# Kernel optimization log

Hardware: AMD Instinct MI355X
Metric: run time of the kernel (lower is better)

Reference implementation:

```python
import jax, jax.numpy as jnp
import numpy as np

DIM = 768
N_HEADS = 12
HEAD_DIM = DIM // N_HEADS
MLP_DIM = 3072
DEPTH = 12
B, N = 16, 512


def setup_inputs() -> dict:
    key = jax.random.key(0)
    ks = jax.random.split(key, 12)
    s = 0.02
    return {
        "x": jax.random.normal(ks[0], (B, N, DIM), dtype=jnp.float32),
        "ln_w": jnp.ones((DIM,), jnp.float32),
        "ln_b": jnp.zeros((DIM,), jnp.float32),
        "wq": jax.random.normal(ks[1], (DIM, DIM), jnp.float32) * s,
        "bq": jnp.zeros((DIM,), jnp.float32),
        "wk": jax.random.normal(ks[2], (DIM, DIM), jnp.float32) * s,
        "bk": jnp.zeros((DIM,), jnp.float32),
        "wv": jax.random.normal(ks[3], (DIM, DIM), jnp.float32) * s,
        "bv": jnp.zeros((DIM,), jnp.float32),
        "w1": jax.random.normal(ks[4], (DIM, MLP_DIM), jnp.float32) * s,
        "b1": jnp.zeros((MLP_DIM,), jnp.float32),
        "w2": jax.random.normal(ks[5], (MLP_DIM, DIM), jnp.float32) * s,
        "b2": jnp.zeros((DIM,), jnp.float32),
    }


def _layernorm(x, w, b):
    mu = jnp.mean(x, axis=-1, keepdims=True)
    var = jnp.var(x, axis=-1, keepdims=True)
    return (x - mu) * jax.lax.rsqrt(var + 1e-5) * w + b


def _mha(x, wq, bq, wk, bk, wv, bv):
    # x: [b, n, dim]; weights stored as [in, out]
    def heads(t):
        return t.reshape(B, N, N_HEADS, HEAD_DIM).transpose(0, 2, 1, 3)  # b h n d
    q = heads(x @ wq + bq)
    k = heads(x @ wk + bk)
    v = heads(x @ wv + bv)
    scores = jnp.einsum('bhqd,bhkd->bhqk', q, k) / np.sqrt(HEAD_DIM).astype(np.float32)
    attn = jax.nn.softmax(scores, axis=-1)
    o = jnp.einsum('bhqk,bhkd->bhqd', attn, v)
    return o.transpose(0, 2, 1, 3).reshape(B, N, DIM)


def reference(x, ln_w, ln_b, wq, bq, wk, bk, wv, bv, w1, b1, w2, b2):
    # Dropout is identity in eval mode. Same weights reused each depth iteration.
    for _ in range(DEPTH):
        x = _mha(_layernorm(x, ln_w, ln_b), wq, bq, wk, bk, wv, bv) + x
        h = _layernorm(x, ln_w, ln_b)
        h = jax.nn.gelu(h @ w1 + b1, approximate=False) @ w2 + b2
        x = h + x
    return x
```

## Files before the change

kernel.cpp:

```cpp
#include <hip/hip_runtime.h>

typedef __bf16 bf16x8 __attribute__((ext_vector_type(8)));
typedef float f32x4 __attribute__((ext_vector_type(4)));
typedef unsigned short ushort8_t __attribute__((ext_vector_type(8)));
typedef unsigned short ushort4_t __attribute__((ext_vector_type(4)));

#define MFMA16(a, b, c) __builtin_amdgcn_mfma_f32_16x16x32_bf16((a), (b), (c), 0, 0, 0)

#define GLOAD16(gp, lp)                                                        \
  __builtin_amdgcn_global_load_lds(                                            \
      (__attribute__((address_space(1))) void*)(gp),                           \
      (__attribute__((address_space(3))) void*)(lp), 16, 0, 0)

__device__ __forceinline__ unsigned short f2bf(float f) {
  unsigned u = __builtin_bit_cast(unsigned, f);
  return (unsigned short)((u + 0x7FFFu + ((u >> 16) & 1u)) >> 16);
}

__global__ __launch_bounds__(256) void transpose_f2b(
    const float* __restrict__ src, unsigned short* __restrict__ dst,
    int Kdim, int Ndim) {
  long i = (long)blockIdx.x * 256 + threadIdx.x;
  if (i >= (long)Kdim * Ndim) return;
  int n = (int)(i / Kdim);
  int kk = (int)(i - (long)n * Kdim);
  dst[i] = f2bf(src[(long)kk * Ndim + n]);
}

__global__ __launch_bounds__(256) void ln_kernel(
    const float* __restrict__ x, const float* __restrict__ gw,
    const float* __restrict__ gb, unsigned short* __restrict__ h) {
  const int row = blockIdx.x * 4 + (threadIdx.x >> 6);
  const int l = threadIdx.x & 63;
  const float* xr = x + (long)row * 768;
  f32x4 va[3];
#pragma unroll
  for (int i = 0; i < 3; i++) va[i] = *(const f32x4*)(xr + i * 256 + l * 4);
  float s = 0.f, ss = 0.f;
#pragma unroll
  for (int i = 0; i < 3; i++)
#pragma unroll
    for (int j = 0; j < 4; j++) {
      float t = va[i][j];
      s += t;
      ss += t * t;
    }
#pragma unroll
  for (int off = 1; off < 64; off <<= 1) {
    s += __shfl_xor(s, off, 64);
    ss += __shfl_xor(ss, off, 64);
  }
  const float mu = s * (1.f / 768.f);
  const float var = ss * (1.f / 768.f) - mu * mu;
  const float inv = rsqrtf(var + 1e-5f);
  unsigned short* hp = h + (long)row * 768;
#pragma unroll
  for (int i = 0; i < 3; i++) {
    f32x4 wv = *(const f32x4*)(gw + i * 256 + l * 4);
    f32x4 bv = *(const f32x4*)(gb + i * 256 + l * 4);
    ushort4_t o;
#pragma unroll
    for (int j = 0; j < 4; j++) o[j] = f2bf((va[i][j] - mu) * inv * wv[j] + bv[j]);
    *(ushort4_t*)(hp + i * 256 + l * 4) = o;
  }
}

enum { EPI_QKV = 0, EPI_GELU = 1, EPI_RES = 2 };

template <int EPI, int MREP>
__global__ __launch_bounds__(256) void gemm_bt(
    const unsigned short* __restrict__ A, const unsigned short* __restrict__ BT,
    int K, const float* __restrict__ bb0, const float* __restrict__ bb1,
    const float* __restrict__ bb2, unsigned short* __restrict__ o0,
    unsigned short* __restrict__ o1, unsigned short* __restrict__ o2,
    const float* oFin, float* oFout) {
  constexpr int BM = MREP * 32;
  constexpr int ABUF = BM * 32;
  __shared__ unsigned short As[2][ABUF];
  __shared__ unsigned short Bs[2][128 * 32];
  const int tid = threadIdx.x;
  const int w = tid >> 6, l = tid & 63;
  const int lr = l & 15, lg = l >> 4;
  const int wr = w >> 1, wc = w & 1;
  const int fchunk = ((l & 3) ^ ((l >> 3) & 3)) * 8;
  const int sR = (lr >> 1) & 3;

  const int nx = gridDim.x;
  const int nwg = nx * gridDim.y;
  int wg = blockIdx.y * nx + blockIdx.x;
  {
    const int qq = nwg >> 3, rr = nwg & 7;
    const int xcd = wg & 7, idx = wg >> 3;
    wg = (xcd < rr ? xcd * (qq + 1) : rr * (qq + 1) + (xcd - rr) * qq) + idx;
  }
  const int bx = wg % nx, by = wg / nx;
  const int m0 = by * BM, n0 = bx * 128;

  const unsigned short* Ag =
      A + (long)(m0 + w * (BM / 4) + (l >> 2)) * K + fchunk;
  const unsigned short* Bg = BT + (long)(n0 + w * 32 + (l >> 2)) * K + fchunk;
  unsigned short* AsW = &As[0][w * (BM / 4) * 32 + l * 8];
  unsigned short* BsW = &Bs[0][w * 1024 + l * 8];

  auto stage = [&](int buf, int kt) {
    const unsigned short* ag = Ag + kt * 32;
    const unsigned short* bg = Bg + kt * 32;
    unsigned short* aw = AsW + buf * ABUF;
    unsigned short* bw = BsW + buf * 4096;
#pragma unroll
    for (int i = 0; i < BM / 64; i++) GLOAD16(ag + i * 16 * K, aw + i * 512);
    GLOAD16(bg, bw);
    GLOAD16(bg + 16 * K, bw + 512);
  };

  f32x4 acc[MREP][4] = {};
  const int nk = K >> 5;
  stage(0, 0);
  __syncthreads();
  for (int kt = 0; kt < nk; ++kt) {
    const int cur = kt & 1;
    if (kt + 1 < nk) stage(cur ^ 1, kt + 1);
    bf16x8 a[MREP], b[4];
#pragma unroll
    for (int i = 0; i < MREP; i++)
      a[i] = *(const bf16x8*)(&As[cur][(wr * MREP * 16 + i * 16 + lr) * 32 +
                                       ((lg ^ sR) * 8)]);
#pragma unroll
    for (int j = 0; j < 4; j++)
      b[j] = *(const bf16x8*)(&Bs[cur][(wc * 64 + j * 16 + lr) * 32 +
                                       ((lg ^ sR) * 8)]);
#pragma unroll
    for (int i = 0; i < MREP; i++)
#pragma unroll
      for (int j = 0; j < 4; j++) acc[i][j] = MFMA16(a[i], b[j], acc[i][j]);
    __syncthreads();
  }

  if (EPI == EPI_QKV) {
    const int whichq = n0 / 768;
    const int cc0 = n0 - whichq * 768;
    const float* bias = whichq == 0 ? bb0 : whichq == 1 ? bb1 : bb2;
    if (whichq < 2) {
      unsigned short* dst = whichq == 0 ? o0 : o1;
#pragma unroll
      for (int i = 0; i < MREP; i++) {
        const int r = m0 + wr * MREP * 16 + i * 16 + lg * 4;
#pragma unroll
        for (int j = 0; j < 4; j++) {
          const int ccol = cc0 + wc * 64 + j * 16 + lr;
          const int hd = ccol >> 6, d = ccol & 63;
          const float bv = bias[ccol];
#pragma unroll
          for (int q = 0; q < 4; q++) {
            const int row = r + q;
            const int bidx = row >> 9, n = row & 511;
            const long addr = ((long)(bidx * 12 + hd) * 512 + n) * 64 + d;
            dst[addr] = f2bf(acc[i][j][q] + bv);
          }
        }
      }
    } else {
#pragma unroll
      for (int i = 0; i < MREP; i++) {
        const int r = m0 + wr * MREP * 16 + i * 16 + lg * 4;
        const int bidx = r >> 9, n = r & 511;
#pragma unroll
        for (int j = 0; j < 4; j++) {
          const int ccol = cc0 + wc * 64 + j * 16 + lr;
          const int hd = ccol >> 6, d = ccol & 63;
          const float bv = bias[ccol];
          ushort4_t pk;
#pragma unroll
          for (int q = 0; q < 4; q++) pk[q] = f2bf(acc[i][j][q] + bv);
          *(ushort4_t*)(&o2[((long)(bidx * 12 + hd) * 64 + d) * 512 + n]) = pk;
        }
      }
    }
  } else if (EPI == EPI_GELU) {
#pragma unroll
    for (int i = 0; i < MREP; i++) {
      const int r = m0 + wr * MREP * 16 + i * 16 + lg * 4;
#pragma unroll
      for (int j = 0; j < 4; j++) {
        const int c = n0 + wc * 64 + j * 16 + lr;
        const float bv = bb0[c];
#pragma unroll
        for (int q = 0; q < 4; q++) {
          float v = acc[i][j][q] + bv;
          const float u = v * (0.7978845608f + 0.0356774081f * v * v);
          const float g = v / (1.0f + __expf(-2.0f * u));
          o0[(long)(r + q) * 3072 + c] = f2bf(g);
        }
      }
    }
  } else {
#pragma unroll
    for (int i = 0; i < MREP; i++) {
      const int r = m0 + wr * MREP * 16 + i * 16 + lg * 4;
#pragma unroll
      for (int j = 0; j < 4; j++) {
        const int c = n0 + wc * 64 + j * 16 + lr;
        const float bv = bb0[c];
#pragma unroll
        for (int q = 0; q < 4; q++) {
          const long addr = (long)(r + q) * 768 + c;
          oFout[addr] = acc[i][j][q] + bv + oFin[addr];
        }
      }
    }
  }
}

__global__ __launch_bounds__(256) void attn_kernel(
    const unsigned short* __restrict__ qg, const unsigned short* __restrict__ kg,
    const unsigned short* __restrict__ vtg, float* __restrict__ x) {
  __shared__ unsigned short Sh[128 * 64];
  __shared__ unsigned short Ks[2][64 * 64];
  __shared__ unsigned short Vt[2][64 * 64];
  const int qt = blockIdx.x, h = blockIdx.y, b = blockIdx.z;
  const int bh = b * 12 + h;
  const int tid = threadIdx.x, w = tid >> 6, l = tid & 63;
  const int lr = l & 15, lg = l >> 4;
  const int fchunk = ((l & 7) ^ ((l >> 3) & 7)) * 8;
  const int rk = lr & 7;

  const unsigned short* qbase =
      qg + ((long)bh * 512 + qt * 128 + w * 32 + (l >> 3)) * 64 + fchunk;
  unsigned short* shW = &Sh[w * 2048 + l * 8];
#pragma unroll
  for (int cc = 0; cc < 4; cc++) GLOAD16(qbase + cc * 8 * 64, shW + cc * 512);

  const unsigned short* kbase =
      kg + ((long)bh * 512 + w * 16 + (l >> 3)) * 64 + fchunk;
  const unsigned short* vbase =
      vtg + ((long)bh * 64 + w * 16 + (l >> 3)) * 512 + fchunk;
  unsigned short* KsW = &Ks[0][w * 1024 + l * 8];
  unsigned short* VtW = &Vt[0][w * 1024 + l * 8];

  auto stageKV = [&](int buf, int kt) {
#pragma unroll
    for (int cc = 0; cc < 2; cc++) {
      GLOAD16(kbase + (kt * 64 + cc * 8) * 64, KsW + buf * 4096 + cc * 512);
      GLOAD16(vbase + cc * 8 * 512 + kt * 64, VtW + buf * 4096 + cc * 512);
    }
  };
  stageKV(0, 0);
  __syncthreads();

  bf16x8 qa[2][2];
#pragma unroll
  for (int mi = 0; mi < 2; mi++)
#pragma unroll
    for (int ds = 0; ds < 2; ds++) {
      qa[mi][ds] = *(const bf16x8*)(&Sh[(w * 32 + mi * 16 + lr) * 64 +
                                        ((ds * 4 + lg) ^ rk) * 8]);
#pragma unroll
      for (int e = 0; e < 8; e++)
        qa[mi][ds][e] = (__bf16)(0.125f * (float)qa[mi][ds][e]);
    }

  unsigned short* Pw = &Sh[w * 2048];
  float lsum[8] = {};
  f32x4 o[2][4] = {};

  for (int kt = 0; kt < 8; ++kt) {
    const int cur = kt & 1;
    if (kt < 7) stageKV(cur ^ 1, kt + 1);

    f32x4 s[2][4] = {};
#pragma unroll
    for (int ds = 0; ds < 2; ++ds) {
      bf16x8 kb[4];
#pragma unroll
      for (int nj = 0; nj < 4; nj++)
        kb[nj] = *(const bf16x8*)(&Ks[cur][(nj * 16 + lr) * 64 +
                                           ((ds * 4 + lg) ^ rk) * 8]);
#pragma unroll
      for (int mi = 0; mi < 2; mi++)
#pragma unroll
        for (int nj = 0; nj < 4; nj++) s[mi][nj] = MFMA16(qa[mi][ds], kb[nj], s[mi][nj]);
    }

#pragma unroll
    for (int mi = 0; mi < 2; mi++)
#pragma unroll
      for (int nj = 0; nj < 4; nj++) {
        const int cL = nj * 2 + (lr >> 3);
#pragma unroll
        for (int q = 0; q < 4; q++) {
          const int row = mi * 16 + lg * 4 + q;
          const float p = __expf(s[mi][nj][q]);
          lsum[mi * 4 + q] += p;
          Pw[row * 64 + ((cL ^ (row & 7)) * 8) + (lr & 7)] = f2bf(p);
        }
      }

#pragma unroll
    for (int ks = 0; ks < 2; ++ks) {
      bf16x8 pa[2], vb[4];
#pragma unroll
      for (int mi = 0; mi < 2; mi++)
        pa[mi] = *(const bf16x8*)(&Pw[(mi * 16 + lr) * 64 +
                                      ((ks * 4 + lg) ^ rk) * 8]);
#pragma unroll
      for (int dj = 0; dj < 4; dj++)
        vb[dj] = *(const bf16x8*)(&Vt[cur][(dj * 16 + lr) * 64 +
                                           ((ks * 4 + lg) ^ rk) * 8]);
#pragma unroll
      for (int mi = 0; mi < 2; mi++)
#pragma unroll
        for (int dj = 0; dj < 4; dj++) o[mi][dj] = MFMA16(pa[mi], vb[dj], o[mi][dj]);
    }
    __syncthreads();
  }

#pragma unroll
  for (int i = 0; i < 8; i++) {
#pragma unroll
    for (int off = 1; off < 16; off <<= 1) lsum[i] += __shfl_xor(lsum[i], off, 64);
  }

#pragma unroll
  for (int mi = 0; mi < 2; mi++) {
#pragma unroll
    for (int q = 0; q < 4; q++) {
      const int n = qt * 128 + w * 32 + mi * 16 + lg * 4 + q;
      const float inv = 1.0f / lsum[mi * 4 + q];
      const long base = ((long)(b * 512 + n)) * 768 + h * 64;
#pragma unroll
      for (int dj = 0; dj < 4; dj++) {
        const long a = base + dj * 16 + lr;
        x[a] = x[a] + o[mi][dj][q] * inv;
      }
    }
  }
}

extern "C" void kernel_launch(void* const* d_in, const int* in_sizes, int n_in,
                              void* d_out, int out_size, void* d_ws,
                              size_t ws_size, hipStream_t stream) {
  const float* x_in = (const float*)d_in[0];
  const float* ln_w = (const float*)d_in[1];
  const float* ln_b = (const float*)d_in[2];
  const float* wq = (const float*)d_in[3];
  const float* bq = (const float*)d_in[4];
  const float* wk = (const float*)d_in[5];
  const float* bk = (const float*)d_in[6];
  const float* wv = (const float*)d_in[7];
  const float* bv = (const float*)d_in[8];
  const float* w1 = (const float*)d_in[9];
  const float* b1 = (const float*)d_in[10];
  const float* w2 = (const float*)d_in[11];
  const float* b2 = (const float*)d_in[12];

  char* p = (char*)d_ws;
  float* xw = (float*)p;            p += 8192L * 768 * 4;
  unsigned short* hbuf = (unsigned short*)p;  p += 8192L * 768 * 2;
  unsigned short* wqkvT = (unsigned short*)p; p += 2304L * 768 * 2;
  unsigned short* w1T = (unsigned short*)p;   p += 3072L * 768 * 2;
  unsigned short* w2T = (unsigned short*)p;   p += 768L * 3072 * 2;
  unsigned short* qb = (unsigned short*)p;
  unsigned short* kb = qb + 6291456L;
  unsigned short* vt = kb + 6291456L;
  unsigned short* gbuf = qb;

  hipMemcpyAsync(xw, x_in, 8192L * 768 * 4, hipMemcpyDeviceToDevice, stream);

  transpose_f2b<<<(768 * 768 + 255) / 256, 256, 0, stream>>>(wq, wqkvT, 768, 768);
  transpose_f2b<<<(768 * 768 + 255) / 256, 256, 0, stream>>>(wk, wqkvT + 589824L, 768, 768);
  transpose_f2b<<<(768 * 768 + 255) / 256, 256, 0, stream>>>(wv, wqkvT + 1179648L, 768, 768);
  transpose_f2b<<<(768 * 3072 + 255) / 256, 256, 0, stream>>>(w1, w1T, 768, 3072);
  transpose_f2b<<<(768 * 3072 + 255) / 256, 256, 0, stream>>>(w2, w2T, 3072, 768);

  for (int layer = 0; layer < 12; ++layer) {
    ln_kernel<<<2048, 256, 0, stream>>>(xw, ln_w, ln_b, hbuf);
    gemm_bt<EPI_QKV, 4><<<dim3(18, 64), 256, 0, stream>>>(
        hbuf, wqkvT, 768, bq, bk, bv, qb, kb, vt, nullptr, nullptr);
    attn_kernel<<<dim3(4, 12, 16), 256, 0, stream>>>(qb, kb, vt, xw);
    ln_kernel<<<2048, 256, 0, stream>>>(xw, ln_w, ln_b, hbuf);
    gemm_bt<EPI_GELU, 4><<<dim3(24, 64), 256, 0, stream>>>(
        hbuf, w1T, 768, b1, nullptr, nullptr, gbuf, nullptr, nullptr, nullptr,
        nullptr);
    gemm_bt<EPI_RES, 2><<<dim3(6, 128), 256, 0, stream>>>(
        gbuf, w2T, 3072, b2, nullptr, nullptr, nullptr, nullptr, nullptr, xw,
        layer == 11 ? (float*)d_out : xw);
  }
}
```

Measured before the change: 2.888 ms.

## Triple-buffer GEMM and attention LDS staging with vmcnt waits and single barrier

```diff
diff --git a/kernel.cpp b/kernel.cpp
--- a/kernel.cpp
+++ b/kernel.cpp
@@ -11,6 +11,12 @@
   __builtin_amdgcn_global_load_lds(                                            \
       (__attribute__((address_space(1))) void*)(gp),                           \
       (__attribute__((address_space(3))) void*)(lp), 16, 0, 0)
+
+#define WAITVM(N) asm volatile("s_waitcnt vmcnt(" #N ")" ::: "memory")
+__device__ __forceinline__ void barrier_fence() {
+  __builtin_amdgcn_s_barrier();
+  __builtin_amdgcn_sched_barrier(0);
+}
 
 __device__ __forceinline__ unsigned short f2bf(float f) {
   unsigned u = __builtin_bit_cast(unsigned, f);
@@ -76,8 +82,9 @@
     const float* oFin, float* oFout) {
   constexpr int BM = MREP * 32;
   constexpr int ABUF = BM * 32;
-  __shared__ unsigned short As[2][ABUF];
-  __shared__ unsigned short Bs[2][128 * 32];
+  constexpr int LPS = BM / 64 + 2;
+  __shared__ unsigned short As[3][ABUF];
+  __shared__ unsigned short Bs[3][128 * 32];
   const int tid = threadIdx.x;
   const int w = tid >> 6, l = tid & 63;
   const int lr = l & 15, lg = l >> 4;
@@ -99,14 +106,12 @@
   const unsigned short* Ag =
       A + (long)(m0 + w * (BM / 4) + (l >> 2)) * K + fchunk;
   const unsigned short* Bg = BT + (long)(n0 + w * 32 + (l >> 2)) * K + fchunk;
-  unsigned short* AsW = &As[0][w * (BM / 4) * 32 + l * 8];
-  unsigned short* BsW = &Bs[0][w * 1024 + l * 8];
 
   auto stage = [&](int buf, int kt) {
     const unsigned short* ag = Ag + kt * 32;
     const unsigned short* bg = Bg + kt * 32;
-    unsigned short* aw = AsW + buf * ABUF;
-    unsigned short* bw = BsW + buf * 4096;
+    unsigned short* aw = &As[buf][w * (BM / 4) * 32 + l * 8];
+    unsigned short* bw = &Bs[buf][w * 1024 + l * 8];
 #pragma unroll
     for (int i = 0; i < BM / 64; i++) GLOAD16(ag + i * 16 * K, aw + i * 512);
     GLOAD16(bg, bw);
@@ -116,10 +121,21 @@
   f32x4 acc[MREP][4] = {};
   const int nk = K >> 5;
   stage(0, 0);
-  __syncthreads();
+  stage(1, 1);
+  int cur = 0;
   for (int kt = 0; kt < nk; ++kt) {
-    const int cur = kt & 1;
-    if (kt + 1 < nk) stage(cur ^ 1, kt + 1);
+    if (kt + 2 < nk) {
+      if constexpr (LPS == 4) WAITVM(4); else WAITVM(3);
+      barrier_fence();
+      const int nxt = cur + 2 >= 3 ? cur - 1 : cur + 2;
+      stage(nxt, kt + 2);
+    } else if (kt + 1 < nk) {
+      if constexpr (LPS == 4) WAITVM(4); else WAITVM(3);
+      barrier_fence();
+    } else {
+      WAITVM(0);
+      barrier_fence();
+    }
     bf16x8 a[MREP], b[4];
 #pragma unroll
     for (int i = 0; i < MREP; i++)
@@ -133,7 +149,7 @@
     for (int i = 0; i < MREP; i++)
 #pragma unroll
       for (int j = 0; j < 4; j++) acc[i][j] = MFMA16(a[i], b[j], acc[i][j]);
-    __syncthreads();
+    cur = cur + 1 >= 3 ? 0 : cur + 1;
   }
 
   if (EPI == EPI_QKV) {
@@ -215,8 +231,8 @@
     const unsigned short* __restrict__ qg, const unsigned short* __restrict__ kg,
     const unsigned short* __restrict__ vtg, float* __restrict__ x) {
   __shared__ unsigned short Sh[128 * 64];
-  __shared__ unsigned short Ks[2][64 * 64];
-  __shared__ unsigned short Vt[2][64 * 64];
+  __shared__ unsigned short Ks[3][64 * 64];
+  __shared__ unsigned short Vt[3][64 * 64];
   const int qt = blockIdx.x, h = blockIdx.y, b = blockIdx.z;
   const int bh = b * 12 + h;
   const int tid = threadIdx.x, w = tid >> 6, l = tid & 63;
@@ -234,19 +250,19 @@
       kg + ((long)bh * 512 + w * 16 + (l >> 3)) * 64 + fchunk;
   const unsigned short* vbase =
       vtg + ((long)bh * 64 + w * 16 + (l >> 3)) * 512 + fchunk;
-  unsigned short* KsW = &Ks[0][w * 1024 + l * 8];
-  unsigned short* VtW = &Vt[0][w * 1024 + l * 8];
 
   auto stageKV = [&](int buf, int kt) {
 #pragma unroll
     for (int cc = 0; cc < 2; cc++) {
-      GLOAD16(kbase + (kt * 64 + cc * 8) * 64, KsW + buf * 4096 + cc * 512);
-      GLOAD16(vbase + cc * 8 * 512 + kt * 64, VtW + buf * 4096 + cc * 512);
+      GLOAD16(kbase + (kt * 64 + cc * 8) * 64, &Ks[buf][w * 1024 + l * 8 + cc * 512]);
+      GLOAD16(vbase + cc * 8 * 512 + kt * 64, &Vt[buf][w * 1024 + l * 8 + cc * 512]);
     }
   };
   stageKV(0, 0);
-  __syncthreads();
-
+  stageKV(1, 1);
+
+  WAITVM(8);
+  __builtin_amdgcn_sched_barrier(0);
   bf16x8 qa[2][2];
 #pragma unroll
   for (int mi = 0; mi < 2; mi++)
@@ -263,9 +279,20 @@
   float lsum[8] = {};
   f32x4 o[2][4] = {};
 
+  int cur = 0;
   for (int kt = 0; kt < 8; ++kt) {
-    const int cur = kt & 1;
-    if (kt < 7) stageKV(cur ^ 1, kt + 1);
+    if (kt + 2 < 8) {
+      WAITVM(4);
+      barrier_fence();
+      const int nxt = cur + 2 >= 3 ? cur - 1 : cur + 2;
+      stageKV(nxt, kt + 2);
+    } else if (kt + 1 < 8) {
+      WAITVM(4);
+      barrier_fence();
+    } else {
+      WAITVM(0);
+      barrier_fence();
+    }
 
     f32x4 s[2][4] = {};
 #pragma unroll
@@ -311,7 +338,7 @@
 #pragma unroll
         for (int dj = 0; dj < 4; dj++) o[mi][dj] = MFMA16(pa[mi], vb[dj], o[mi][dj]);
     }
-    __syncthreads();
+    cur = cur + 1 >= 3 ? 0 : cur + 1;
   }
 
 #pragma unroll
```

Result: slower. 2.996 ms (+3.7%).

## Use 256x256-tile register-staged GEMM for QKV and MLP-up projections

Applied to the files above, without the earlier changes.

```diff
diff --git a/kernel.cpp b/kernel.cpp
--- a/kernel.cpp
+++ b/kernel.cpp
@@ -11,6 +11,9 @@
   __builtin_amdgcn_global_load_lds(                                            \
       (__attribute__((address_space(1))) void*)(gp),                           \
       (__attribute__((address_space(3))) void*)(lp), 16, 0, 0)
+
+#define WAITVM(N) asm volatile("s_waitcnt vmcnt(" #N ")" ::: "memory")
+#define WAITLGKM0 asm volatile("s_waitcnt lgkmcnt(0)" ::: "memory")
 
 __device__ __forceinline__ unsigned short f2bf(float f) {
   unsigned u = __builtin_bit_cast(unsigned, f);
@@ -67,14 +70,178 @@
 
 enum { EPI_QKV = 0, EPI_GELU = 1, EPI_RES = 2 };
 
-template <int EPI, int MREP>
-__global__ __launch_bounds__(256) void gemm_bt(
+template <int EPI>
+__global__ __launch_bounds__(512) void gemm256(
     const unsigned short* __restrict__ A, const unsigned short* __restrict__ BT,
     int K, const float* __restrict__ bb0, const float* __restrict__ bb1,
     const float* __restrict__ bb2, unsigned short* __restrict__ o0,
-    unsigned short* __restrict__ o1, unsigned short* __restrict__ o2,
-    const float* oFin, float* oFout) {
-  constexpr int BM = MREP * 32;
+    unsigned short* __restrict__ o1, unsigned short* __restrict__ o2) {
+  __shared__ unsigned short As[2][2][8192];
+  __shared__ unsigned short Bs[2][2][8192];
+  const int tid = threadIdx.x;
+  const int w = tid >> 6, l = tid & 63;
+  const int lr = l & 15, lg = l >> 4;
+  const int wr = w >> 2, wc = w & 3;
+  const int sK = (lr >> 1) & 3;
+
+  const int nx = gridDim.x;
+  const int nwg = nx * gridDim.y;
+  int wg = blockIdx.y * nx + blockIdx.x;
+  {
+    const int qq = nwg >> 3, rr = nwg & 7;
+    const int xcd = wg & 7, idx = wg >> 3;
+    wg = (xcd < rr ? xcd * (qq + 1) : rr * (qq + 1) + (xcd - rr) * qq) + idx;
+  }
+  const int bx = wg % nx, by = wg / nx;
+  const int m0 = by * 256, n0 = bx * 256;
+
+  const int srow = tid >> 2;
+  const int schunk = tid & 3;
+  const int spos = schunk ^ ((tid >> 3) & 3);
+
+  ushort8_t rgA[2][2], rgB[2][2];
+
+  auto ldA = [&](int kt, int kk, ushort8_t (&rg)[2]) {
+#pragma unroll
+    for (int r2 = 0; r2 < 2; r2++)
+      rg[r2] = *(const ushort8_t*)(A + (long)(m0 + r2 * 128 + srow) * K +
+                                   kt * 64 + kk * 32 + schunk * 8);
+  };
+  auto ldB = [&](int kt, int kk, ushort8_t (&rg)[2]) {
+#pragma unroll
+    for (int r2 = 0; r2 < 2; r2++)
+      rg[r2] = *(const ushort8_t*)(BT + (long)(n0 + r2 * 128 + srow) * K +
+                                   kt * 64 + kk * 32 + schunk * 8);
+  };
+  auto wrA = [&](int s, int kk, ushort8_t (&rg)[2]) {
+#pragma unroll
+    for (int r2 = 0; r2 < 2; r2++)
+      *(ushort8_t*)&As[s][kk][(r2 * 128 + srow) * 32 + spos * 8] = rg[r2];
+  };
+  auto wrB = [&](int s, int kk, ushort8_t (&rg)[2]) {
+#pragma unroll
+    for (int r2 = 0; r2 < 2; r2++)
+      *(ushort8_t*)&Bs[s][kk][(r2 * 128 + srow) * 32 + spos * 8] = rg[r2];
+  };
+
+  f32x4 acc[8][4] = {};
+  const int NT = K >> 6;
+
+  ldA(0, 0, rgA[0]); ldB(0, 0, rgB[0]);
+  ldA(0, 1, rgA[1]); ldB(0, 1, rgB[1]);
+  WAITVM(4);
+  wrA(0, 0, rgA[0]); wrB(0, 0, rgB[0]);
+  ldA(1, 0, rgA[0]); ldB(1, 0, rgB[0]);
+  WAITVM(4);
+  wrA(0, 1, rgA[1]); wrB(0, 1, rgB[1]);
+  ldA(1, 1, rgA[1]); ldB(1, 1, rgB[1]);
+
+  for (int kt = 0; kt < NT; ++kt) {
+    const int s = kt & 1;
+#pragma unroll
+    for (int kk = 0; kk < 2; ++kk) {
+      if (kt < NT - 2) {
+        WAITVM(4);
+      } else if (kt == NT - 2) {
+        if (kk == 0) { WAITVM(4); } else { WAITVM(0); }
+      }
+      if (kt + 1 < NT) {
+        wrA(s ^ 1, kk, rgA[kk]);
+        wrB(s ^ 1, kk, rgB[kk]);
+      }
+      if (kt + 2 < NT) {
+        ldA(kt + 2, kk, rgA[kk]);
+        ldB(kt + 2, kk, rgB[kk]);
+      }
+      WAITLGKM0;
+      __builtin_amdgcn_sched_barrier(0);
+      __builtin_amdgcn_s_barrier();
+      __builtin_amdgcn_sched_barrier(0);
+      bf16x8 b[4];
+#pragma unroll
+      for (int j = 0; j < 4; j++)
+        b[j] = *(const bf16x8*)&Bs[s][kk][(wc * 64 + j * 16 + lr) * 32 +
+                                          ((lg ^ sK) * 8)];
+#pragma unroll
+      for (int H = 0; H < 2; H++) {
+        bf16x8 a[4];
+#pragma unroll
+        for (int i = 0; i < 4; i++)
+          a[i] = *(const bf16x8*)&As[s][kk][(wr * 128 + H * 64 + i * 16 + lr) * 32 +
+                                            ((lg ^ sK) * 8)];
+        __builtin_amdgcn_s_setprio(1);
+#pragma unroll
+        for (int i = 0; i < 4; i++)
+#pragma unroll
+          for (int j = 0; j < 4; j++)
+            acc[H * 4 + i][j] = MFMA16(a[i], b[j], acc[H * 4 + i][j]);
+        __builtin_amdgcn_s_setprio(0);
+      }
+    }
+  }
+
+  if (EPI == EPI_QKV) {
+    const int whichq = n0 / 768;
+    const int cc0 = n0 - whichq * 768 + wc * 64;
+    const float* bias = whichq == 0 ? bb0 : whichq == 1 ? bb1 : bb2;
+    if (whichq < 2) {
+      unsigned short* dst = whichq == 0 ? o0 : o1;
+#pragma unroll
+      for (int fm = 0; fm < 8; fm++) {
+        const int r = m0 + wr * 128 + fm * 16 + lg * 4;
+        const int bidx = r >> 9, nb = r & 511;
+#pragma unroll
+        for (int fn = 0; fn < 4; fn++) {
+          const int cc = cc0 + fn * 16 + lr;
+          const int hd = cc >> 6, d = cc & 63;
+          const float bv = bias[cc];
+          unsigned short* pp = &dst[((long)(bidx * 12 + hd) * 512 + nb) * 64 + d];
+#pragma unroll
+          for (int q = 0; q < 4; q++) pp[q * 64] = f2bf(acc[fm][fn][q] + bv);
+        }
+      }
+    } else {
+#pragma unroll
+      for (int fm = 0; fm < 8; fm++) {
+        const int r = m0 + wr * 128 + fm * 16 + lg * 4;
+        const int bidx = r >> 9, nb = r & 511;
+#pragma unroll
+        for (int fn = 0; fn < 4; fn++) {
+          const int cc = cc0 + fn * 16 + lr;
+          const int hd = cc >> 6, d = cc & 63;
+          const float bv = bias[cc];
+          ushort4_t pk;
+#pragma unroll
+          for (int q = 0; q < 4; q++) pk[q] = f2bf(acc[fm][fn][q] + bv);
+          *(ushort4_t*)(&o2[((long)(bidx * 12 + hd) * 64 + d) * 512 + nb]) = pk;
+        }
+      }
+    }
+  } else {
+#pragma unroll
+    for (int fm = 0; fm < 8; fm++) {
+      const int r = m0 + wr * 128 + fm * 16 + lg * 4;
+#pragma unroll
+      for (int fn = 0; fn < 4; fn++) {
+        const int c = n0 + wc * 64 + fn * 16 + lr;
+        const float bv = bb0[c];
+#pragma unroll
+        for (int q = 0; q < 4; q++) {
+          float v = acc[fm][fn][q] + bv;
+          const float u = v * (0.7978845608f + 0.0356774081f * v * v);
+          const float g = v / (1.0f + __expf(-2.0f * u));
+          o0[(long)(r + q) * 3072 + c] = f2bf(g);
+        }
+      }
+    }
+  }
+}
+
+__global__ __launch_bounds__(256) void gemm_res(
+    const unsigned short* __restrict__ A, const unsigned short* __restrict__ BT,
+    int K, const float* __restrict__ bb0, const float* __restrict__ oFin,
+    float* __restrict__ oFout) {
+  constexpr int BM = 64;
   constexpr int ABUF = BM * 32;
   __shared__ unsigned short As[2][ABUF];
   __shared__ unsigned short Bs[2][128 * 32];
@@ -82,8 +249,6 @@
   const int w = tid >> 6, l = tid & 63;
   const int lr = l & 15, lg = l >> 4;
   const int wr = w >> 1, wc = w & 1;
-  const int fchunk = ((l & 3) ^ ((l >> 3) & 3)) * 8;
-  const int sR = (lr >> 1) & 3;
 
   const int nx = gridDim.x;
   const int nwg = nx * gridDim.y;
@@ -96,116 +261,51 @@
   const int bx = wg % nx, by = wg / nx;
   const int m0 = by * BM, n0 = bx * 128;
 
-  const unsigned short* Ag =
-      A + (long)(m0 + w * (BM / 4) + (l >> 2)) * K + fchunk;
-  const unsigned short* Bg = BT + (long)(n0 + w * 32 + (l >> 2)) * K + fchunk;
-  unsigned short* AsW = &As[0][w * (BM / 4) * 32 + l * 8];
+  const unsigned short* Ag = A + (long)(m0 + w * 16 + (l >> 2)) * K + (l & 3) * 8;
+  const unsigned short* Bg = BT + (long)(n0 + w * 32 + (l >> 2)) * K + (l & 3) * 8;
+  unsigned short* AsW = &As[0][w * 16 * 32 + l * 8];
   unsigned short* BsW = &Bs[0][w * 1024 + l * 8];
 
   auto stage = [&](int buf, int kt) {
     const unsigned short* ag = Ag + kt * 32;
     const unsigned short* bg = Bg + kt * 32;
-    unsigned short* aw = AsW + buf * ABUF;
-    unsigned short* bw = BsW + buf * 4096;
-#pragma unroll
-    for (int i = 0; i < BM / 64; i++) GLOAD16(ag + i * 16 * K, aw + i * 512);
-    GLOAD16(bg, bw);
-    GLOAD16(bg + 16 * K, bw + 512);
-  };
-
-  f32x4 acc[MREP][4] = {};
+    GLOAD16(ag, AsW + buf * ABUF);
+    GLOAD16(bg, BsW + buf * 4096);
+    GLOAD16(bg + 16 * K, BsW + buf * 4096 + 512);
+  };
+
+  f32x4 acc[2][4] = {};
   const int nk = K >> 5;
   stage(0, 0);
   __syncthreads();
   for (int kt = 0; kt < nk; ++kt) {
     const int cur = kt & 1;
     if (kt + 1 < nk) stage(cur ^ 1, kt + 1);
-    bf16x8 a[MREP], b[4];
-#pragma unroll
-    for (int i = 0; i < MREP; i++)
-      a[i] = *(const bf16x8*)(&As[cur][(wr * MREP * 16 + i * 16 + lr) * 32 +
-                                       ((lg ^ sR) * 8)]);
+    bf16x8 a[2], b[4];
+#pragma unroll
+    for (int i = 0; i < 2; i++)
+      a[i] = *(const bf16x8*)(&As[cur][(wr * 32 + i * 16 + lr) * 32 + lg * 8]);
 #pragma unroll
     for (int j = 0; j < 4; j++)
-      b[j] = *(const bf16x8*)(&Bs[cur][(wc * 64 + j * 16 + lr) * 32 +
-                                       ((lg ^ sR) * 8)]);
-#pragma unroll
-    for (int i = 0; i < MREP; i++)
+      b[j] = *(const bf16x8*)(&Bs[cur][(wc * 64 + j * 16 + lr) * 32 + lg * 8]);
+#pragma unroll
+    for (int i = 0; i < 2; i++)
 #pragma unroll
       for (int j = 0; j < 4; j++) acc[i][j] = MFMA16(a[i], b[j], acc[i][j]);
     __syncthreads();
   }
 
-  if (EPI == EPI_QKV) {
-    const int whichq = n0 / 768;
-    const int cc0 = n0 - whichq * 768;
-    const float* bias = whichq == 0 ? bb0 : whichq == 1 ? bb1 : bb2;
-    if (whichq < 2) {
-      unsigned short* dst = whichq == 0 ? o0 : o1;
-#pragma unroll
-      for (int i = 0; i < MREP; i++) {
-        const int r = m0 + wr * MREP * 16 + i * 16 + lg * 4;
-#pragma unroll
-        for (int j = 0; j < 4; j++) {
-          const int ccol = cc0 + wc * 64 + j * 16 + lr;
-          const int hd = ccol >> 6, d = ccol & 63;
-          const float bv = bias[ccol];
-#pragma unroll
-          for (int q = 0; q < 4; q++) {
-            const int row = r + q;
-            const int bidx = row >> 9, n = row & 511;
-            const long addr = ((long)(bidx * 12 + hd) * 512 + n) * 64 + d;
-            dst[addr] = f2bf(acc[i][j][q] + bv);
-          }
-        }
-      }
-    } else {
-#pragma unroll
-      for (int i = 0; i < MREP; i++) {
-        const int r = m0 + wr * MREP * 16 + i * 16 + lg * 4;
-        const int bidx = r >> 9, n = r & 511;
-#pragma unroll
-        for (int j = 0; j < 4; j++) {
-          const int ccol = cc0 + wc * 64 + j * 16 + lr;
-          const int hd = ccol >> 6, d = ccol & 63;
-          const float bv = bias[ccol];
-          ushort4_t pk;
-#pragma unroll
-          for (int q = 0; q < 4; q++) pk[q] = f2bf(acc[i][j][q] + bv);
-          *(ushort4_t*)(&o2[((long)(bidx * 12 + hd) * 64 + d) * 512 + n]) = pk;
-        }
-      }
-    }
-  } else if (EPI == EPI_GELU) {
-#pragma unroll
-    for (int i = 0; i < MREP; i++) {
-      const int r = m0 + wr * MREP * 16 + i * 16 + lg * 4;
-#pragma unroll
-      for (int j = 0; j < 4; j++) {
-        const int c = n0 + wc * 64 + j * 16 + lr;
-        const float bv = bb0[c];
-#pragma unroll
-        for (int q = 0; q < 4; q++) {
-          float v = acc[i][j][q] + bv;
-          const float u = v * (0.7978845608f + 0.0356774081f * v * v);
-          const float g = v / (1.0f + __expf(-2.0f * u));
-          o0[(long)(r + q) * 3072 + c] = f2bf(g);
-        }
-      }
-    }
-  } else {
-#pragma unroll
-    for (int i = 0; i < MREP; i++) {
-      const int r = m0 + wr * MREP * 16 + i * 16 + lg * 4;
-#pragma unroll
-      for (int j = 0; j < 4; j++) {
-        const int c = n0 + wc * 64 + j * 16 + lr;
-        const float bv = bb0[c];
-#pragma unroll
-        for (int q = 0; q < 4; q++) {
-          const long addr = (long)(r + q) * 768 + c;
-          oFout[addr] = acc[i][j][q] + bv + oFin[addr];
-        }
+#pragma unroll
+  for (int i = 0; i < 2; i++) {
+    const int r = m0 + wr * 32 + i * 16 + lg * 4;
+#pragma unroll
+    for (int j = 0; j < 4; j++) {
+      const int c = n0 + wc * 64 + j * 16 + lr;
+      const float bv = bb0[c];
+#pragma unroll
+      for (int q = 0; q < 4; q++) {
+        const long addr = (long)(r + q) * 768 + c;
+        oFout[addr] = acc[i][j][q] + bv + oFin[addr];
       }
     }
   }
@@ -374,15 +474,13 @@
 
   for (int layer = 0; layer < 12; ++layer) {
     ln_kernel<<<2048, 256, 0, stream>>>(xw, ln_w, ln_b, hbuf);
-    gemm_bt<EPI_QKV, 4><<<dim3(18, 64), 256, 0, stream>>>(
-        hbuf, wqkvT, 768, bq, bk, bv, qb, kb, vt, nullptr, nullptr);
+    gemm256<EPI_QKV><<<dim3(9, 32), 512, 0, stream>>>(
+        hbuf, wqkvT, 768, bq, bk, bv, qb, kb, vt);
     attn_kernel<<<dim3(4, 12, 16), 256, 0, stream>>>(qb, kb, vt, xw);
     ln_kernel<<<2048, 256, 0, stream>>>(xw, ln_w, ln_b, hbuf);
-    gemm_bt<EPI_GELU, 4><<<dim3(24, 64), 256, 0, stream>>>(
-        hbuf, w1T, 768, b1, nullptr, nullptr, gbuf, nullptr, nullptr, nullptr,
-        nullptr);
-    gemm_bt<EPI_RES, 2><<<dim3(6, 128), 256, 0, stream>>>(
-        gbuf, w2T, 3072, b2, nullptr, nullptr, nullptr, nullptr, nullptr, xw,
-        layer == 11 ? (float*)d_out : xw);
-  }
-}
+    gemm256<EPI_GELU><<<dim3(12, 32), 512, 0, stream>>>(
+        hbuf, w1T, 768, b1, nullptr, nullptr, gbuf, nullptr, nullptr);
+    gemm_res<<<dim3(6, 128), 256, 0, stream>>>(
+        gbuf, w2T, 3072, b2, xw, layer == 11 ? (float*)d_out : xw);
+  }
+}
```

New measurement: 2.814 ms. 1.03x faster.

## Deepen GEMM K-step to 64 with two LDS sub-tiles and MFMA priority

Applied to the files above, without the earlier changes.

```diff
diff --git a/kernel.cpp b/kernel.cpp
--- a/kernel.cpp
+++ b/kernel.cpp
@@ -75,15 +75,12 @@
     unsigned short* __restrict__ o1, unsigned short* __restrict__ o2,
     const float* oFin, float* oFout) {
   constexpr int BM = MREP * 32;
-  constexpr int ABUF = BM * 32;
-  __shared__ unsigned short As[2][ABUF];
-  __shared__ unsigned short Bs[2][128 * 32];
+  __shared__ unsigned short As[2][2][BM * 32];
+  __shared__ unsigned short Bs[2][2][128 * 32];
   const int tid = threadIdx.x;
   const int w = tid >> 6, l = tid & 63;
   const int lr = l & 15, lg = l >> 4;
   const int wr = w >> 1, wc = w & 1;
-  const int fchunk = ((l & 3) ^ ((l >> 3) & 3)) * 8;
-  const int sR = (lr >> 1) & 3;
 
   const int nx = gridDim.x;
   const int nwg = nx * gridDim.y;
@@ -96,44 +93,47 @@
   const int bx = wg % nx, by = wg / nx;
   const int m0 = by * BM, n0 = bx * 128;
 
-  const unsigned short* Ag =
-      A + (long)(m0 + w * (BM / 4) + (l >> 2)) * K + fchunk;
-  const unsigned short* Bg = BT + (long)(n0 + w * 32 + (l >> 2)) * K + fchunk;
-  unsigned short* AsW = &As[0][w * (BM / 4) * 32 + l * 8];
-  unsigned short* BsW = &Bs[0][w * 1024 + l * 8];
+  const unsigned short* Ag = A + (long)(m0 + w * (BM / 4) + (l >> 2)) * K + (l & 3) * 8;
+  const unsigned short* Bg = BT + (long)(n0 + w * 32 + (l >> 2)) * K + (l & 3) * 8;
 
   auto stage = [&](int buf, int kt) {
-    const unsigned short* ag = Ag + kt * 32;
-    const unsigned short* bg = Bg + kt * 32;
-    unsigned short* aw = AsW + buf * ABUF;
-    unsigned short* bw = BsW + buf * 4096;
-#pragma unroll
-    for (int i = 0; i < BM / 64; i++) GLOAD16(ag + i * 16 * K, aw + i * 512);
-    GLOAD16(bg, bw);
-    GLOAD16(bg + 16 * K, bw + 512);
+    const long ko = (long)kt * 64;
+#pragma unroll
+    for (int kk = 0; kk < 2; kk++) {
+#pragma unroll
+      for (int h = 0; h < BM / 64; h++)
+        GLOAD16(Ag + (long)(h * 16) * K + ko + kk * 32,
+                &As[buf][kk][(w * (BM / 4) + h * 16) * 32 + l * 8]);
+#pragma unroll
+      for (int h = 0; h < 2; h++)
+        GLOAD16(Bg + (long)(h * 16) * K + ko + kk * 32,
+                &Bs[buf][kk][(w * 32 + h * 16) * 32 + l * 8]);
+    }
   };
 
   f32x4 acc[MREP][4] = {};
-  const int nk = K >> 5;
+  const int nk = K >> 6;
   stage(0, 0);
-  __syncthreads();
   for (int kt = 0; kt < nk; ++kt) {
     const int cur = kt & 1;
+    __syncthreads();
     if (kt + 1 < nk) stage(cur ^ 1, kt + 1);
-    bf16x8 a[MREP], b[4];
-#pragma unroll
-    for (int i = 0; i < MREP; i++)
-      a[i] = *(const bf16x8*)(&As[cur][(wr * MREP * 16 + i * 16 + lr) * 32 +
-                                       ((lg ^ sR) * 8)]);
-#pragma unroll
-    for (int j = 0; j < 4; j++)
-      b[j] = *(const bf16x8*)(&Bs[cur][(wc * 64 + j * 16 + lr) * 32 +
-                                       ((lg ^ sR) * 8)]);
-#pragma unroll
-    for (int i = 0; i < MREP; i++)
-#pragma unroll
-      for (int j = 0; j < 4; j++) acc[i][j] = MFMA16(a[i], b[j], acc[i][j]);
-    __syncthreads();
+#pragma unroll
+    for (int kk = 0; kk < 2; kk++) {
+      bf16x8 a[MREP], b[4];
+#pragma unroll
+      for (int i = 0; i < MREP; i++)
+        a[i] = *(const bf16x8*)(&As[cur][kk][(wr * MREP * 16 + i * 16 + lr) * 32 + lg * 8]);
+#pragma unroll
+      for (int j = 0; j < 4; j++)
+        b[j] = *(const bf16x8*)(&Bs[cur][kk][(wc * 64 + j * 16 + lr) * 32 + lg * 8]);
+      __builtin_amdgcn_s_setprio(1);
+#pragma unroll
+      for (int i = 0; i < MREP; i++)
+#pragma unroll
+        for (int j = 0; j < 4; j++) acc[i][j] = MFMA16(a[i], b[j], acc[i][j]);
+      __builtin_amdgcn_s_setprio(0);
+    }
   }
 
   if (EPI == EPI_QKV) {
@@ -163,7 +163,7 @@
 #pragma unroll
       for (int i = 0; i < MREP; i++) {
         const int r = m0 + wr * MREP * 16 + i * 16 + lg * 4;
-        const int bidx = r >> 9, n = r & 511;
+        const int bidx = r >> 9, nb = r & 511;
 #pragma unroll
         for (int j = 0; j < 4; j++) {
           const int ccol = cc0 + wc * 64 + j * 16 + lr;
@@ -172,7 +172,7 @@
           ushort4_t pk;
 #pragma unroll
           for (int q = 0; q < 4; q++) pk[q] = f2bf(acc[i][j][q] + bv);
-          *(ushort4_t*)(&o2[((long)(bidx * 12 + hd) * 64 + d) * 512 + n]) = pk;
+          *(ushort4_t*)(&o2[((long)(bidx * 12 + hd) * 64 + d) * 512 + nb]) = pk;
         }
       }
     }
```

Result: faster. 2.697 ms (-6.6%).
